# Kernel tuning notes

Measured on AMD Instinct MI355X. Metric: run time of the kernel, lower is better.

## Reference

```python
import jax, jax.numpy as jnp
import numpy as np

B, S, HID = 1, 2048, 2048
NH, NKV, HD = 32, 8, 64
SCALE = HD ** -0.5


def _rotary_tables(seq_len, dim, base=10000.0):
    inv_freq = 1.0 / (base ** (jnp.arange(0, dim, 2, dtype=jnp.float32) / dim))
    t = jnp.arange(seq_len, dtype=jnp.float32)
    freqs = jnp.outer(t, inv_freq)                      # [S, D/2]
    emb = jnp.concatenate([freqs, freqs], axis=-1)      # [S, D]
    return jnp.cos(emb)[None], jnp.sin(emb)[None]       # [1, S, D]


def setup_inputs() -> dict:
    key = jax.random.key(0)
    ks = jax.random.split(key, 5)
    cos, sin = _rotary_tables(S, HD)
    std = HID ** -0.5
    return {
        "hidden_states": jax.random.normal(ks[0], (B, S, HID), jnp.float32),
        "cos": cos,
        "sin": sin,
        "Wq": jax.random.normal(ks[1], (HID, NH * HD), jnp.float32) * std,
        "Wk": jax.random.normal(ks[2], (HID, NKV * HD), jnp.float32) * std,
        "Wv": jax.random.normal(ks[3], (HID, NKV * HD), jnp.float32) * std,
        "Wo": jax.random.normal(ks[4], (NH * HD, HID), jnp.float32) * std,
    }


def _rotate_half(x):
    x1, x2 = jnp.split(x, 2, axis=-1)
    return jnp.concatenate([-x2, x1], axis=-1)


def reference(hidden_states, cos, sin, Wq, Wk, Wv, Wo):
    b, s, _ = hidden_states.shape
    # projections -> [B, H, S, D]
    q = (hidden_states @ Wq).reshape(b, s, NH, HD).transpose(0, 2, 1, 3)
    k = (hidden_states @ Wk).reshape(b, s, NKV, HD).transpose(0, 2, 1, 3)
    v = (hidden_states @ Wv).reshape(b, s, NKV, HD).transpose(0, 2, 1, 3)
    # rotary embedding (broadcast over heads)
    c = cos[:, None, :, :]
    sn = sin[:, None, :, :]
    q = q * c + _rotate_half(q) * sn
    k = k * c + _rotate_half(k) * sn
    # GQA: repeat kv heads
    groups = NH // NKV
    k = jnp.repeat(k, groups, axis=1)
    v = jnp.repeat(v, groups, axis=1)
    scores = jnp.einsum("bhqd,bhkd->bhqk", q, k) * SCALE
    causal = jnp.tril(jnp.ones((s, s), dtype=bool))
    scores = jnp.where(causal, scores, jnp.finfo(scores.dtype).min)
    weights = jax.nn.softmax(scores, axis=-1)
    attn = jnp.einsum("bhqk,bhkd->bhqd", weights, v)
    attn = attn.transpose(0, 2, 1, 3).reshape(b, s, NH * HD)
    out = attn @ Wo
    return out, weights
```

## Files before the change

kernel.cpp:

```cpp
#include <hip/hip_runtime.h>

typedef short short8 __attribute__((ext_vector_type(8)));
typedef float f32x4 __attribute__((ext_vector_type(4)));

#define S_LEN 2048
#define HID 2048
#define NH 32
#define NKV 8
#define HD 64
#define DQKV 3072
#define SCALE 0.125f
#define SM_OFF 8.0f

static __device__ __forceinline__ unsigned short f2bf(float f) {
    unsigned int u = __float_as_uint(f);
    u += 0x7FFF + ((u >> 16) & 1);
    return (unsigned short)(u >> 16);
}
static __device__ __forceinline__ float bf2f(unsigned short u) {
    return __uint_as_float((unsigned int)u << 16);
}

#define GLDS16(g, l)                                                                     \
    __builtin_amdgcn_global_load_lds((const __attribute__((address_space(1))) unsigned int*)(g), \
                                     (__attribute__((address_space(3))) unsigned int*)(l), 16, 0, 0)

__global__ void prep(const float* __restrict__ Wq, const float* __restrict__ Wk,
                     const float* __restrict__ Wv, const float* __restrict__ Wo,
                     const float* __restrict__ hidden,
                     unsigned short* __restrict__ Wt, unsigned short* __restrict__ Wot,
                     unsigned short* __restrict__ Hb) {
    const int z = blockIdx.z;
    const int t = threadIdx.x;
    if (z == 4) {
        int idx = (blockIdx.y * 64 + blockIdx.x) * 256 + t;
        float4 v = ((const float4*)hidden)[idx];
        ushort4 o = {f2bf(v.x), f2bf(v.y), f2bf(v.z), f2bf(v.w)};
        ((ushort4*)Hb)[idx] = o;
        return;
    }
    const float* src; unsigned short* dst; int sld;
    if (z == 0)      { src = Wq; dst = Wt; sld = HID; }
    else if (z == 1) { if (blockIdx.x >= 16) return; src = Wk; dst = Wt + (size_t)2048 * HID; sld = 512; }
    else if (z == 2) { if (blockIdx.x >= 16) return; src = Wv; dst = Wt + (size_t)2560 * HID; sld = 512; }
    else             { src = Wo; dst = Wot; sld = HID; }
    __shared__ float tile[32][33];
    const int tx = t & 31, ty = t >> 5;
    const int r0 = blockIdx.y * 32, c0 = blockIdx.x * 32;
#pragma unroll
    for (int i = 0; i < 4; ++i)
        tile[ty * 4 + i][tx] = src[(size_t)(r0 + ty * 4 + i) * sld + c0 + tx];
    __syncthreads();
#pragma unroll
    for (int i = 0; i < 4; ++i)
        dst[(size_t)(c0 + ty * 4 + i) * HID + r0 + tx] = f2bf(tile[tx][ty * 4 + i]);
}

template <int MODE>
__global__ __launch_bounds__(512) void gemm_fused(const unsigned short* __restrict__ A,
                                                  const unsigned short* __restrict__ Bt,
                                                  float* __restrict__ C,
                                                  const float* __restrict__ cosb,
                                                  const float* __restrict__ sinb,
                                                  unsigned short* __restrict__ Qb,
                                                  unsigned short* __restrict__ Kb,
                                                  unsigned short* __restrict__ Vt,
                                                  int K, int lda, int ldb, int ldc) {
    __shared__ __align__(16) unsigned short As[128 * 64];
    __shared__ __align__(16) unsigned short Bs[128 * 64];
    const int t = threadIdx.x, lane = t & 63, wv = t >> 6;
    const int m0 = blockIdx.y * 128, n0 = blockIdx.x * 128;
    const int wm = wv >> 1, wn = wv & 1;
    const int lr = lane & 15, lg = lane >> 4;
    const int srow = lane >> 3;
    const int scol = ((lane & 7) ^ srow) * 8;
    f32x4 acc[2][4] = {};
    for (int k0 = 0; k0 < K; k0 += 64) {
        __syncthreads();
#pragma unroll
        for (int p = 0; p < 2; ++p) {
            int rbase = wv * 16 + p * 8;
            GLDS16(&A[(size_t)(m0 + rbase + srow) * lda + k0 + scol], &As[rbase * 64]);
            GLDS16(&Bt[(size_t)(n0 + rbase + srow) * ldb + k0 + scol], &Bs[rbase * 64]);
        }
        __syncthreads();
#pragma unroll
        for (int kk = 0; kk < 2; ++kk) {
            short8 a[2], b[4];
#pragma unroll
            for (int i = 0; i < 2; ++i) {
                int row = wm * 32 + i * 16 + lr;
                a[i] = *(const short8*)&As[row * 64 + (((kk * 4 + lg) ^ (row & 7)) * 8)];
            }
#pragma unroll
            for (int j = 0; j < 4; ++j) {
                int row = wn * 64 + j * 16 + lr;
                b[j] = *(const short8*)&Bs[row * 64 + (((kk * 4 + lg) ^ (row & 7)) * 8)];
            }
#pragma unroll
            for (int i = 0; i < 2; ++i)
#pragma unroll
                for (int j = 0; j < 4; ++j)
                    acc[i][j] = __builtin_amdgcn_mfma_f32_16x16x32_bf16(a[i], b[j], acc[i][j], 0, 0, 0);
        }
    }

    if (MODE == 1) {
#pragma unroll
        for (int i = 0; i < 2; ++i)
#pragma unroll
            for (int j = 0; j < 4; ++j)
#pragma unroll
                for (int r = 0; r < 4; ++r)
                    C[(size_t)(m0 + wm * 32 + i * 16 + lg * 4 + r) * ldc +
                      n0 + wn * 64 + j * 16 + lr] = acc[i][j][r];
        return;
    }

    const int head = (n0 + wn * 64) >> 6;
    if (head < NH + NKV) {
        unsigned short* dst = (head < NH) ? Qb : Kb;
        const int dld = (head < NH) ? HID : 512;
        const int hc = (head < NH) ? head * HD : (head - NH) * HD;
#pragma unroll
        for (int i = 0; i < 2; ++i) {
            const int s0 = m0 + wm * 32 + i * 16 + lg * 4;
#pragma unroll
            for (int j = 0; j < 2; ++j) {
                const int c = j * 16 + lr;
#pragma unroll
                for (int r = 0; r < 4; ++r) {
                    const int s = s0 + r;
                    float x1 = acc[i][j][r], x2 = acc[i][j + 2][r];
                    float c1 = cosb[s * HD + c],      s1 = sinb[s * HD + c];
                    float c2 = cosb[s * HD + c + 32], s2 = sinb[s * HD + c + 32];
                    dst[(size_t)s * dld + hc + c]      = f2bf(x1 * c1 - x2 * s1);
                    dst[(size_t)s * dld + hc + c + 32] = f2bf(x2 * c2 + x1 * s2);
                }
            }
        }
    } else {
        const int vh = head - NH - NKV;
#pragma unroll
        for (int i = 0; i < 2; ++i) {
            const int s0 = m0 + wm * 32 + i * 16 + lg * 4;
#pragma unroll
            for (int j = 0; j < 4; ++j) {
                const int d = vh * HD + j * 16 + lr;
                ushort4 o = {f2bf(acc[i][j][0]), f2bf(acc[i][j][1]),
                             f2bf(acc[i][j][2]), f2bf(acc[i][j][3])};
                *(ushort4*)&Vt[(size_t)d * S_LEN + s0] = o;
            }
        }
    }
}

#define KSZ (128 * 72)
#define VSZ (64 * 136)
__global__ __launch_bounds__(512) void attn_fused(const unsigned short* __restrict__ Qb,
                                                  const unsigned short* __restrict__ Kb,
                                                  const unsigned short* __restrict__ Vt,
                                                  float* __restrict__ w,
                                                  unsigned short* __restrict__ Ab) {
    __shared__ __align__(16) unsigned short Ks[2 * KSZ];
    __shared__ __align__(16) unsigned short Vs[2 * VSZ];
    __shared__ __align__(16) unsigned short Ps[8][32 * 40];
    const int p = blockIdx.x, h = blockIdx.y, kvh = h >> 2;
    const int t = threadIdx.x, lane = t & 63, wv = t >> 6;
    const int grp = wv & 1, wr = wv >> 1;
    const int qt = grp ? (15 - p) : p;
    const int q0 = qt * 128;
    const int lr = lane & 15, lg = lane >> 4;
    const int ktmax = 15 - p;
    unsigned short* Pw = &Ps[wv][0];

    const float C1 = SCALE;
    const float NEG = -1.0e30f;

    short8 qf[2][2];
#pragma unroll
    for (int i = 0; i < 2; ++i)
#pragma unroll
        for (int kk = 0; kk < 2; ++kk)
            qf[i][kk] = *(const short8*)&Qb[(size_t)(q0 + wr * 32 + i * 16 + lr) * HID +
                                            h * HD + kk * 32 + lg * 8];

    const int krow = t >> 2, kc = (t & 3) * 16;
    const int vrow = t >> 3, vc = (t & 7) * 16;

    short8 kA, kB, vA, vB;
#define LOADK(kt) { const unsigned short* kp = &Kb[(size_t)((kt) * 128 + krow) * 512 + kvh * HD]; \
                    kA = *(const short8*)&kp[kc]; kB = *(const short8*)&kp[kc + 8]; }
#define WRITEK(b) { *(short8*)&Ks[(b) * KSZ + krow * 72 + kc] = kA;                 \
                    *(short8*)&Ks[(b) * KSZ + krow * 72 + kc + 8] = kB; }
#define LOADV(kt) { const unsigned short* vp = &Vt[(size_t)(kvh * HD + vrow) * S_LEN + (kt) * 128]; \
                    vA = *(const short8*)&vp[vc]; vB = *(const short8*)&vp[vc + 8]; }
#define WRITEV(b) { *(short8*)&Vs[(b) * VSZ + vrow * 136 + vc] = vA;                \
                    *(short8*)&Vs[(b) * VSZ + vrow * 136 + vc + 8] = vB; }
#define ZEROTILE(kt) {                                                              \
        f32x4 z4 = {0.f, 0.f, 0.f, 0.f};                                            \
        for (int rr = 0; rr < 16; ++rr) {                                           \
            int row = wr * 32 + rr * 2 + (lane >> 5);                               \
            *(f32x4*)&w[((size_t)h * S_LEN + q0 + row) * S_LEN + (kt) * 128 + (lane & 31) * 4] = z4; \
        }                                                                           \
    }

    float l_r[2] = {0.f, 0.f};

    LOADK(0); WRITEK(0);
    __syncthreads();
    LOADK(1);
    for (int kt = 0; kt <= ktmax; ++kt) {
        const int b = kt & 1;
        if (kt <= qt) {
            f32x4 acc[8][2] = {};
#pragma unroll
            for (int kk = 0; kk < 2; ++kk) {
                short8 af[8];
#pragma unroll
                for (int j = 0; j < 8; ++j)
                    af[j] = *(const short8*)&Ks[b * KSZ + (j * 16 + lr) * 72 + kk * 32 + lg * 8];
#pragma unroll
                for (int j = 0; j < 8; ++j)
#pragma unroll
                    for (int i = 0; i < 2; ++i)
                        acc[j][i] = __builtin_amdgcn_mfma_f32_16x16x32_bf16(af[j], qf[i][kk], acc[j][i], 0, 0, 0);
            }
            const bool diag = (kt == qt);
#pragma unroll
            for (int i = 0; i < 2; ++i) {
                const int qg = q0 + wr * 32 + i * 16 + lr;
                float sum = 0.f;
#pragma unroll
                for (int j = 0; j < 8; ++j)
#pragma unroll
                    for (int r = 0; r < 4; ++r) {
                        int kg = kt * 128 + j * 16 + lg * 4 + r;
                        float s2 = fmaf(acc[j][i][r], C1, -SM_OFF);
                        s2 = (!diag || kg <= qg) ? s2 : NEG;
                        sum += __expf(s2);
                    }
                sum += __shfl_xor(sum, 16);
                sum += __shfl_xor(sum, 32);
                l_r[i] += sum;
            }
        } else {
            ZEROTILE(kt);
        }
        if (kt < ktmax) WRITEK(b ^ 1);
        __syncthreads();
        if (kt + 2 <= ktmax) LOADK(kt + 2);
    }
    for (int kt = ktmax + 1; kt < 16; ++kt) ZEROTILE(kt);

    const float invl[2] = {1.f / l_r[0], 1.f / l_r[1]};

    f32x4 o[2][4] = {};
    LOADK(0); LOADV(0); WRITEK(0); WRITEV(0);
    __syncthreads();
    LOADK(1); LOADV(1);
    for (int kt = 0; kt <= ktmax; ++kt) {
        const int b = kt & 1;
        if (kt <= qt) {
            f32x4 acc[8][2] = {};
#pragma unroll
            for (int kk = 0; kk < 2; ++kk) {
                short8 af[8];
#pragma unroll
                for (int j = 0; j < 8; ++j)
                    af[j] = *(const short8*)&Ks[b * KSZ + (j * 16 + lr) * 72 + kk * 32 + lg * 8];
#pragma unroll
                for (int j = 0; j < 8; ++j)
#pragma unroll
                    for (int i = 0; i < 2; ++i)
                        acc[j][i] = __builtin_amdgcn_mfma_f32_16x16x32_bf16(af[j], qf[i][kk], acc[j][i], 0, 0, 0);
            }
            const bool diag = (kt == qt);
#pragma unroll
            for (int ks = 0; ks < 4; ++ks) {
#pragma unroll
                for (int i = 0; i < 2; ++i) {
                    const int qg = q0 + wr * 32 + i * 16 + lr;
#pragma unroll
                    for (int jj = 0; jj < 2; ++jj) {
                        const int j = ks * 2 + jj;
                        ushort4 pk;
#pragma unroll
                        for (int r = 0; r < 4; ++r) {
                            int kg = kt * 128 + j * 16 + lg * 4 + r;
                            float s2 = fmaf(acc[j][i][r], C1, -SM_OFF);
                            s2 = (!diag || kg <= qg) ? s2 : NEG;
                            ((unsigned short*)&pk)[r] = f2bf(__expf(s2) * invl[i]);
                        }
                        *(ushort4*)&Pw[(i * 16 + lr) * 40 + jj * 16 + lg * 4] = pk;
                    }
                }
                short8 pa[2], vb[4];
#pragma unroll
                for (int i = 0; i < 2; ++i)
                    pa[i] = *(const short8*)&Pw[(i * 16 + lr) * 40 + lg * 8];
#pragma unroll
                for (int j2 = 0; j2 < 4; ++j2)
                    vb[j2] = *(const short8*)&Vs[b * VSZ + (j2 * 16 + lr) * 136 + ks * 32 + lg * 8];
#pragma unroll
                for (int i = 0; i < 2; ++i)
#pragma unroll
                    for (int j2 = 0; j2 < 4; ++j2)
                        o[i][j2] = __builtin_amdgcn_mfma_f32_16x16x32_bf16(pa[i], vb[j2], o[i][j2], 0, 0, 0);
#pragma unroll
                for (int rp = 0; rp < 2; ++rp) {
                    int rq = (lane >> 2) + rp * 16;
                    int cb = (lane & 3) * 8;
                    short8 pv8 = *(const short8*)&Pw[rq * 40 + cb];
                    f32x4 f0 = {bf2f((unsigned short)pv8[0]), bf2f((unsigned short)pv8[1]),
                                bf2f((unsigned short)pv8[2]), bf2f((unsigned short)pv8[3])};
                    f32x4 f1 = {bf2f((unsigned short)pv8[4]), bf2f((unsigned short)pv8[5]),
                                bf2f((unsigned short)pv8[6]), bf2f((unsigned short)pv8[7])};
                    size_t base = ((size_t)h * S_LEN + q0 + wr * 32 + rq) * S_LEN + kt * 128 + ks * 32 + cb;
                    *(f32x4*)&w[base] = f0;
                    *(f32x4*)&w[base + 4] = f1;
                }
            }
        }
        if (kt < ktmax) { WRITEK(b ^ 1); WRITEV(b ^ 1); }
        __syncthreads();
        if (kt + 2 <= ktmax) { LOADK(kt + 2); LOADV(kt + 2); }
    }
#pragma unroll
    for (int i = 0; i < 2; ++i)
#pragma unroll
        for (int j2 = 0; j2 < 4; ++j2)
#pragma unroll
            for (int r = 0; r < 4; ++r)
                Ab[(size_t)(q0 + wr * 32 + i * 16 + lg * 4 + r) * HID +
                   h * HD + j2 * 16 + lr] = f2bf(o[i][j2][r]);
}

extern "C" void kernel_launch(void* const* d_in, const int* in_sizes, int n_in,
                              void* d_out, int out_size, void* d_ws, size_t ws_size,
                              hipStream_t stream) {
    const float* hidden = (const float*)d_in[0];
    const float* cosb   = (const float*)d_in[1];
    const float* sinb   = (const float*)d_in[2];
    const float* Wq     = (const float*)d_in[3];
    const float* Wk     = (const float*)d_in[4];
    const float* Wv     = (const float*)d_in[5];
    const float* Wo     = (const float*)d_in[6];

    float* out_mat = (float*)d_out;
    float* weights = (float*)d_out + (size_t)S_LEN * HID;

    char* wsb = (char*)d_ws;
    unsigned short* Hb  = (unsigned short*)wsb;
    unsigned short* Wt  = (unsigned short*)(wsb + (size_t)8  * 1024 * 1024);
    unsigned short* Wot = (unsigned short*)(wsb + (size_t)20 * 1024 * 1024);
    unsigned short* Qb  = (unsigned short*)(wsb + (size_t)28 * 1024 * 1024);
    unsigned short* Kb  = (unsigned short*)(wsb + (size_t)36 * 1024 * 1024);
    unsigned short* Vt  = (unsigned short*)(wsb + (size_t)38 * 1024 * 1024);
    unsigned short* Ab  = (unsigned short*)(wsb + (size_t)40 * 1024 * 1024);

    prep<<<dim3(64, 64, 5), 256, 0, stream>>>(Wq, Wk, Wv, Wo, hidden, Wt, Wot, Hb);

    gemm_fused<0><<<dim3(DQKV / 128, S_LEN / 128), 512, 0, stream>>>(
        Hb, Wt, nullptr, cosb, sinb, Qb, Kb, Vt, HID, HID, HID, 0);

    attn_fused<<<dim3(8, NH), 512, 0, stream>>>(Qb, Kb, Vt, weights, Ab);

    gemm_fused<1><<<dim3(HID / 128, S_LEN / 128), 512, 0, stream>>>(
        Ab, Wot, out_mat, nullptr, nullptr, nullptr, nullptr, nullptr, HID, HID, HID, HID);
}
```

Before: 245.9 us.

## Move causal-masked zero fill of attention weights into QKV GEMM kernel

Removes the zeroing of fully masked upper-triangle weight tiles from the attention kernel and instead has each QKV projection GEMM block zero ten such tiles, interleaved across its K-loop iterations. The goal is to overlap the large store-bound zero fill with the compute-bound projection GEMM and to relieve the attention kernel's imbalanced tail work. The cost is extra memory traffic competing with the GEMM's operand loads, and the work mapping is hardcoded to the grid size.

```diff
diff --git a/kernel.cpp b/kernel.cpp
--- a/kernel.cpp
+++ b/kernel.cpp
@@ -65,6 +65,7 @@
                                                   unsigned short* __restrict__ Qb,
                                                   unsigned short* __restrict__ Kb,
                                                   unsigned short* __restrict__ Vt,
+                                                  float* __restrict__ wz,
                                                   int K, int lda, int ldb, int ldc) {
     __shared__ __align__(16) unsigned short As[128 * 64];
     __shared__ __align__(16) unsigned short Bs[128 * 64];
@@ -74,6 +75,7 @@
     const int lr = lane & 15, lg = lane >> 4;
     const int srow = lane >> 3;
     const int scol = ((lane & 7) ^ srow) * 8;
+    const int bid = blockIdx.y * gridDim.x + blockIdx.x;
     f32x4 acc[2][4] = {};
     for (int k0 = 0; k0 < K; k0 += 64) {
         __syncthreads();
@@ -84,6 +86,22 @@
             GLDS16(&Bt[(size_t)(n0 + rbase + srow) * ldb + k0 + scol], &Bs[rbase * 64]);
         }
         __syncthreads();
+        if (MODE == 0) {
+            const int n_it = k0 >> 6;
+            if (n_it < 30 && (n_it % 3) == 0) {
+                int gidx = bid * 10 + n_it / 3;
+                int h = gidx / 120;
+                int tri = gidx - h * 120;
+                int q = 0;
+                while (tri >= 15 - q) { tri -= 15 - q; ++q; }
+                int kt = q + 1 + tri;
+                float* zb = wz + ((size_t)h * S_LEN + q * 128 + (t >> 2)) * S_LEN + kt * 128 + (t & 3) * 4;
+                f32x4 z = {0.f, 0.f, 0.f, 0.f};
+#pragma unroll
+                for (int slot = 0; slot < 8; ++slot)
+                    *(f32x4*)(zb + slot * 16) = z;
+            }
+        }
 #pragma unroll
         for (int kk = 0; kk < 2; ++kk) {
             short8 a[2], b[4];
@@ -197,13 +215,6 @@
                     vA = *(const short8*)&vp[vc]; vB = *(const short8*)&vp[vc + 8]; }
 #define WRITEV(b) { *(short8*)&Vs[(b) * VSZ + vrow * 136 + vc] = vA;                \
                     *(short8*)&Vs[(b) * VSZ + vrow * 136 + vc + 8] = vB; }
-#define ZEROTILE(kt) {                                                              \
-        f32x4 z4 = {0.f, 0.f, 0.f, 0.f};                                            \
-        for (int rr = 0; rr < 16; ++rr) {                                           \
-            int row = wr * 32 + rr * 2 + (lane >> 5);                               \
-            *(f32x4*)&w[((size_t)h * S_LEN + q0 + row) * S_LEN + (kt) * 128 + (lane & 31) * 4] = z4; \
-        }                                                                           \
-    }
 
     float l_r[2] = {0.f, 0.f};
 
@@ -244,14 +255,11 @@
                 sum += __shfl_xor(sum, 32);
                 l_r[i] += sum;
             }
-        } else {
-            ZEROTILE(kt);
         }
         if (kt < ktmax) WRITEK(b ^ 1);
         __syncthreads();
         if (kt + 2 <= ktmax) LOADK(kt + 2);
     }
-    for (int kt = ktmax + 1; kt < 16; ++kt) ZEROTILE(kt);
 
     const float invl[2] = {1.f / l_r[0], 1.f / l_r[1]};
 
@@ -362,10 +370,10 @@
     prep<<<dim3(64, 64, 5), 256, 0, stream>>>(Wq, Wk, Wv, Wo, hidden, Wt, Wot, Hb);
 
     gemm_fused<0><<<dim3(DQKV / 128, S_LEN / 128), 512, 0, stream>>>(
-        Hb, Wt, nullptr, cosb, sinb, Qb, Kb, Vt, HID, HID, HID, 0);
+        Hb, Wt, nullptr, cosb, sinb, Qb, Kb, Vt, weights, HID, HID, HID, 0);
 
     attn_fused<<<dim3(8, NH), 512, 0, stream>>>(Qb, Kb, Vt, weights, Ab);
 
     gemm_fused<1><<<dim3(HID / 128, S_LEN / 128), 512, 0, stream>>>(
-        Ab, Wot, out_mat, nullptr, nullptr, nullptr, nullptr, nullptr, HID, HID, HID, HID);
-}
+        Ab, Wot, out_mat, nullptr, nullptr, nullptr, nullptr, nullptr, nullptr, HID, HID, HID, HID);
+}
```

New measurement: 267.0 us. 8.6% more time.
